# Optimization experiments

Hardware: AMD Instinct MI355X
Metric: run time of the kernel (lower is better)

The kernel has to match this reference:

```python
import jax, jax.numpy as jnp
import numpy as np

D_MODEL, N_LEVELS, N_HEADS, N_POINTS = 256, 4, 8, 4
SHAPES = [(100, 100), (50, 50), (25, 25), (13, 13)]  # (H, W) per level


def setup_inputs() -> dict:
    key = jax.random.key(0)
    ks = jax.random.split(key, 8)
    N = 2
    C = D_MODEL
    Len_in = sum(h * w for h, w in SHAPES)
    Lq = Len_in  # encoder self-attention
    query = jax.random.normal(ks[0], (N, Lq, C), jnp.float32)
    reference_points = jax.random.uniform(ks[1], (N, Lq, N_LEVELS, 2), dtype=jnp.float32)
    input_flatten = jax.random.normal(ks[2], (N, Len_in, C), jnp.float32)
    input_spatial_shapes = np.array(SHAPES, dtype=np.int64)
    areas = input_spatial_shapes[:, 0] * input_spatial_shapes[:, 1]
    input_level_start_index = np.concatenate([[0], np.cumsum(areas)[:-1]]).astype(np.int64)
    s = 1.0 / np.sqrt(C)
    Wv = jax.random.uniform(ks[3], (C, C), jnp.float32, -s, s)
    bv = jnp.zeros((C,), jnp.float32)
    # sampling_offsets: small random weight + the module's grid bias init
    Woff = jax.random.normal(ks[4], (N_HEADS * N_LEVELS * N_POINTS * 2, C), jnp.float32) * 0.01
    thetas = jnp.arange(N_HEADS, dtype=jnp.float32) * (2.0 * np.pi / N_HEADS)
    grid = jnp.stack([jnp.cos(thetas), jnp.sin(thetas)], -1)  # (M,2)
    grid = grid / jnp.max(jnp.abs(grid), axis=-1, keepdims=True)
    grid = jnp.tile(grid[:, None, None, :], (1, N_LEVELS, N_POINTS, 1))
    grid = grid * (jnp.arange(N_POINTS, dtype=jnp.float32) + 1.0)[None, None, :, None]
    boff = grid.reshape(-1)
    Wa = jax.random.normal(ks[5], (N_HEADS * N_LEVELS * N_POINTS, C), jnp.float32) * 0.02
    ba = jnp.zeros((N_HEADS * N_LEVELS * N_POINTS,), jnp.float32)
    Wo = jax.random.uniform(ks[6], (C, C), jnp.float32, -s, s)
    bo = jnp.zeros((C,), jnp.float32)
    return {
        'query': query, 'reference_points': reference_points, 'input_flatten': input_flatten,
        'input_spatial_shapes': input_spatial_shapes, 'input_level_start_index': input_level_start_index,
        'Wv': Wv, 'bv': bv, 'Woff': Woff, 'boff': boff, 'Wa': Wa, 'ba': ba, 'Wo': Wo, 'bo': bo,
    }


def _msda_forward(query, reference_points, input_flatten, shapes, starts,
                  Wv, bv, Woff, boff, Wa, ba, Wo, bo):
    N, Lq, C = query.shape
    M, L, P = N_HEADS, N_LEVELS, N_POINTS
    D = C // M
    value = (input_flatten @ Wv.T + bv).reshape(N, -1, M, D)  # (N, Len_in, M, D)
    off = (query @ Woff.T + boff).reshape(N, Lq, M, L, P, 2)
    attn = jax.nn.softmax((query @ Wa.T + ba).reshape(N, Lq, M, L * P), axis=-1)
    attn = attn.reshape(N, Lq, M, L, P)
    # offset_normalizer = (W_l, H_l)
    norm = jnp.asarray(shapes[:, ::-1].copy(), jnp.float32)  # (L, 2)
    loc = reference_points[:, :, None, :, None, :] + off / norm[None, None, None, :, None, :]
    grids = 2.0 * loc - 1.0  # (N, Lq, M, L, P, 2), grid_sample convention
    out = jnp.zeros((N, Lq, M, D), query.dtype)
    for l in range(L):
        H, W = int(shapes[l, 0]), int(shapes[l, 1])
        s0 = int(starts[l])
        v = value[:, s0:s0 + H * W]  # (N, H*W, M, D)
        # align_corners=False unnormalization
        gx = ((grids[:, :, :, l, :, 0] + 1.0) * W - 1.0) / 2.0  # (N, Lq, M, P)
        gy = ((grids[:, :, :, l, :, 1] + 1.0) * H - 1.0) / 2.0
        x0 = jnp.floor(gx); y0 = jnp.floor(gy)
        fx = gx - x0;       fy = gy - y0
        x0i = x0.astype(jnp.int32); y0i = y0.astype(jnp.int32)

        def gather(iy, ix):
            valid = (iy >= 0) & (iy < H) & (ix >= 0) & (ix < W)
            lin = jnp.clip(iy, 0, H - 1) * W + jnp.clip(ix, 0, W - 1)  # (N, Lq, M, P)
            lin2 = lin.transpose(0, 1, 3, 2).reshape(N, Lq * P, M)
            g = jnp.take_along_axis(v, lin2[..., None], axis=1)  # (N, Lq*P, M, D)
            g = g.reshape(N, Lq, P, M, D).transpose(0, 1, 3, 2, 4)  # (N, Lq, M, P, D)
            return g * valid[..., None]  # zero padding outside

        s00 = gather(y0i, x0i)
        s01 = gather(y0i, x0i + 1)
        s10 = gather(y0i + 1, x0i)
        s11 = gather(y0i + 1, x0i + 1)
        sampled = (s00 * ((1 - fy) * (1 - fx))[..., None] + s01 * ((1 - fy) * fx)[..., None]
                   + s10 * (fy * (1 - fx))[..., None] + s11 * (fy * fx)[..., None])
        out = out + jnp.einsum('nqmp,nqmpd->nqmd', attn[:, :, :, l], sampled)
    out = out.reshape(N, Lq, C)
    return out @ Wo.T + bo


def reference(query, reference_points, input_flatten, input_spatial_shapes, input_level_start_index,
              Wv, bv, Woff, boff, Wa, ba, Wo, bo):
    shapes = np.asarray(input_spatial_shapes)
    starts = np.asarray(input_level_start_index)
    return _msda_forward(query, reference_points, input_flatten, shapes, starts,
                         Wv, bv, Woff, boff, Wa, ba, Wo, bo)
```

## Files before the change

### kernel.cpp

```cpp
#include <hip/hip_runtime.h>
#include <math.h>

#define NB   2
#define LQ   13294
#define NROWS (NB*LQ)
#define CDIM 256
#define HSLICES (NROWS + 1)
#define HS32 ((size_t)HSLICES * 32)

typedef unsigned short u16;
typedef unsigned int   u32;
typedef short bf16x8 __attribute__((ext_vector_type(8)));
typedef float f32x4  __attribute__((ext_vector_type(4)));
typedef float f32x2  __attribute__((ext_vector_type(2)));

struct alignas(8) U16x4 { u16 x, y, z, w; };

__device__ __forceinline__ u16 f2bf(float f) {
    u32 u = __builtin_bit_cast(u32, f);
    u += 0x7FFFu + ((u >> 16) & 1u);
    return (u16)(u >> 16);
}

__device__ __forceinline__ void gload_lds16(const void* g, void* l) {
    __builtin_amdgcn_global_load_lds(
        (__attribute__((address_space(1))) void*)g,
        (__attribute__((address_space(3))) void*)l, 16, 0, 0);
}

__device__ __forceinline__ f32x2 bfpair(u32 u) {
    union { u32 w[2]; f32x2 v; } x;
    x.w[0] = u << 16;
    x.w[1] = u & 0xFFFF0000u;
    return x.v;
}

__global__ __launch_bounds__(256)
void prep_all(const float4* __restrict__ query, const float4* __restrict__ inflat,
              const float* __restrict__ Wv, const float* __restrict__ Woff,
              const float* __restrict__ Wa, const float* __restrict__ Wo,
              u16* __restrict__ qb, u16* __restrict__ ib,
              u16* __restrict__ wb) {
    const int b = blockIdx.x;
    const int t = threadIdx.x;
    if (b < 6647) {
        int i = b * 256 + t;
        float4 v = query[i];
        U16x4 o{f2bf(v.x), f2bf(v.y), f2bf(v.z), f2bf(v.w)};
        *(U16x4*)&qb[(size_t)i * 4] = o;
    } else if (b < 13294) {
        int i = (b - 6647) * 256 + t;
        float4 v = inflat[i];
        U16x4 o{f2bf(v.x), f2bf(v.y), f2bf(v.z), f2bf(v.w)};
        *(U16x4*)&ib[(size_t)i * 4] = o;
    } else {
        int i = (b - 13294) * 256 + t;
        float v;
        if      (i <  65536) v = Wv[i];
        else if (i < 131072) v = Woff[i - 65536];
        else if (i < 163840) v = Wa[i - 131072];
        else                 v = Wo[i - 163840];
        wb[i] = f2bf(v);
    }
}

__device__ __forceinline__ void gemm_core128(
    const u16* __restrict__ A, const u16* __restrict__ Bw, int M, int row0,
    u16* As, u16* Bs, f32x4 (&acc)[4][4]) {
    const int tid  = threadIdx.x;
    const int lane = tid & 63;
    const int wave = tid >> 6;
    const int ln16 = lane & 15;
    const int kq   = lane >> 4;
    const int wr   = (wave >> 1) * 64;
    const int wc   = (wave & 1) * 64;

    #pragma unroll
    for (int kt = 0; kt < 4; ++kt) {
        const int k0 = kt * 64;
        #pragma unroll
        for (int it = 0; it < 4; ++it) {
            int chunk = it * 256 + tid;
            int row = chunk >> 3;
            int ch  = chunk & 7;
            int chs = (ch ^ (row & 7)) * 8;
            int gra = min(row0 + row, M - 1);
            gload_lds16(A  + (size_t)gra * 256 + k0 + chs, As + chunk * 8);
            gload_lds16(Bw + (size_t)row * 256 + k0 + chs, Bs + chunk * 8);
        }
        __syncthreads();
        #pragma unroll
        for (int kf = 0; kf < 2; ++kf) {
            const int ck = kf * 4 + kq;
            bf16x8 a[4], b[4];
            #pragma unroll
            for (int i = 0; i < 4; ++i) {
                int r = wr + i * 16 + ln16;
                a[i] = *(const bf16x8*)&As[r * 64 + ((ck ^ (r & 7)) * 8)];
                int c = wc + i * 16 + ln16;
                b[i] = *(const bf16x8*)&Bs[c * 64 + ((ck ^ (c & 7)) * 8)];
            }
            #pragma unroll
            for (int i = 0; i < 4; ++i)
                #pragma unroll
                for (int j = 0; j < 4; ++j)
                    acc[i][j] = __builtin_amdgcn_mfma_f32_16x16x32_bf16(
                        a[i], b[j], acc[i][j], 0, 0, 0);
        }
        __syncthreads();
    }
}

__global__ __launch_bounds__(256, 4)
void gemm_front(const u16* __restrict__ qb, const u16* __restrict__ ib,
                const u16* __restrict__ wb, const float* __restrict__ bv,
                const float* __restrict__ boff, const float* __restrict__ ba,
                u16* __restrict__ value, float* __restrict__ offb,
                float* __restrict__ logit, int M) {
    __shared__ u16 Sh[128 * 128];
    u16* As = Sh;
    u16* Bs = Sh + 8192;
    const int s    = blockIdx.x;
    const int row0 = blockIdx.y * 128;
    const u16* A  = (s < 2) ? ib : qb;
    const u16* Bw = wb + (size_t)s * 32768;
    const float* bias = (s == 0) ? bv
                      : (s == 1) ? bv + 128
                      : (s == 2) ? boff
                      : (s == 3) ? boff + 128
                      : ba;

    f32x4 acc[4][4] = {};
    gemm_core128(A, Bw, M, row0, As, Bs, acc);

    const int tid  = threadIdx.x;
    const int lane = tid & 63;
    const int wave = tid >> 6;
    const int ln16 = lane & 15, kq = lane >> 4;
    const int wr = (wave >> 1) * 64, wc = (wave & 1) * 64;

    if (s < 2) {
        #pragma unroll
        for (int j = 0; j < 4; ++j) {
            int cl = wc + j * 16 + ln16;
            float bj = bias[cl];
            #pragma unroll
            for (int i = 0; i < 4; ++i)
                #pragma unroll
                for (int r = 0; r < 4; ++r) {
                    int rl = wr + i * 16 + kq * 4 + r;
                    Sh[rl * 128 + cl] = f2bf(acc[i][j][r] + bj);
                }
        }
        __syncthreads();
        #pragma unroll
        for (int it = 0; it < 8; ++it) {
            int ci = it * 256 + tid;
            int tr = ci >> 4;
            int cc = ci & 15;
            int gr = row0 + tr;
            if (gr < M) {
                int cg = s * 128 + cc * 8;
                u16* dst = value + (size_t)(cg >> 5) * HS32
                                 + (size_t)gr * 32 + (cg & 31);
                *(uint4*)dst = *(const uint4*)&Sh[tr * 128 + cc * 8];
            }
        }
        if (s == 0 && blockIdx.y == 0) {
            value[(size_t)(tid >> 5) * HS32 + (size_t)NROWS * 32 + (tid & 31)] = 0;
        }
    } else {
        #pragma unroll
        for (int j = 0; j < 4; ++j) {
            int lc = wc + j * 16 + ln16;
            float bj = bias[lc];
            #pragma unroll
            for (int i = 0; i < 4; ++i) {
                #pragma unroll
                for (int r = 0; r < 4; ++r) {
                    int gr = row0 + wr + i * 16 + kq * 4 + r;
                    if (gr < M) {
                        float o = acc[i][j][r] + bj;
                        if (s < 4)
                            offb[(size_t)gr * 256 + (s - 2) * 128 + lc] = o;
                        else
                            logit[(size_t)gr * 128 + lc] = o;
                    }
                }
            }
        }
    }
}

__global__ __launch_bounds__(256, 4)
void gemm_out(const u16* __restrict__ A, const u16* __restrict__ Bw0,
              const float* __restrict__ bias, float* __restrict__ C, int M) {
    __shared__ u16 Sh[128 * 128];
    u16* As = Sh;
    u16* Bs = Sh + 8192;
    const int s    = blockIdx.x;
    const int row0 = blockIdx.y * 128;
    const u16* Bw = Bw0 + (size_t)s * 32768;

    f32x4 acc[4][4] = {};
    gemm_core128(A, Bw, M, row0, As, Bs, acc);

    const int lane = threadIdx.x & 63;
    const int wave = threadIdx.x >> 6;
    const int ln16 = lane & 15, kq = lane >> 4;
    const int wr = (wave >> 1) * 64, wc = (wave & 1) * 64;
    #pragma unroll
    for (int j = 0; j < 4; ++j) {
        int gc = s * 128 + wc + j * 16 + ln16;
        float bj = bias[gc];
        #pragma unroll
        for (int i = 0; i < 4; ++i) {
            #pragma unroll
            for (int r = 0; r < 4; ++r) {
                int gr = row0 + wr + i * 16 + kq * 4 + r;
                if (gr < M) C[(size_t)gr * 256 + gc] = acc[i][j][r] + bj;
            }
        }
    }
}

__global__ __launch_bounds__(256)
void msda_sample(const u16* __restrict__ value,
                 const float* __restrict__ refpts,
                 const float* __restrict__ off,
                 const float* __restrict__ logits,
                 u16* __restrict__ tmp) {
    __shared__ float sAw[4][8][16];
    __shared__ int   sLin[4][8][16][2];
    __shared__ float sW[4][8][16][4];

    const int t  = threadIdx.x;
    const int qb = blockIdx.x * 4;

    if (t < 32) {
        const int qi = t >> 3, m = t & 7;
        const float* lg = logits + (size_t)(qb + qi) * 128 + m * 16;
        float e[16];
        float mx = -1e30f;
        #pragma unroll
        for (int i = 0; i < 16; ++i) { e[i] = lg[i]; mx = fmaxf(mx, e[i]); }
        float s = 0.f;
        #pragma unroll
        for (int i = 0; i < 16; ++i) { e[i] = __expf(e[i] - mx); s += e[i]; }
        const float inv = 1.f / s;
        #pragma unroll
        for (int i = 0; i < 16; ++i) sAw[qi][m][i] = e[i] * inv;
    }
    __syncthreads();

    #pragma unroll
    for (int j2 = 0; j2 < 2; ++j2) {
        const int job = t + j2 * 256;
        const int qi = job >> 7;
        const int m  = (job >> 4) & 7;
        const int p  = job & 15;
        const int l  = p >> 2, pp = p & 3;
        const int q  = qb + qi;
        const int n  = (q >= LQ) ? 1 : 0;

        const int W = (l == 0) ? 100 : (l == 1) ? 50 : (l == 2) ? 25 : 13;
        const int H = W;
        const int st = (l == 0) ? 0 : (l == 1) ? 10000 : (l == 2) ? 12500 : 13125;
        const float invW = (l == 0) ? 0.01f : (l == 1) ? 0.02f
                         : (l == 2) ? 0.04f : (1.f / 13.f);

        const float rx = refpts[(size_t)q * 8 + l * 2 + 0];
        const float ry = refpts[(size_t)q * 8 + l * 2 + 1];
        const float ox = off[(size_t)q * 256 + m * 32 + (l * 4 + pp) * 2 + 0];
        const float oy = off[(size_t)q * 256 + m * 32 + (l * 4 + pp) * 2 + 1];

        const float locx = rx + ox * invW;
        const float locy = ry + oy * invW;
        const float grx = 2.f * locx - 1.f;
        const float gry = 2.f * locy - 1.f;
        const float gx = ((grx + 1.f) * (float)W - 1.f) * 0.5f;
        const float gy = ((gry + 1.f) * (float)H - 1.f) * 0.5f;
        const float x0f = floorf(gx), y0f = floorf(gy);
        const float fx = gx - x0f, fy = gy - y0f;
        const int x0 = (int)x0f, y0 = (int)y0f;
        const int x1 = x0 + 1, y1 = y0 + 1;

        const int cx0 = min(max(x0, 0), W - 1);
        const int cy0 = min(max(y0, 0), H - 1);
        const int cy1 = min(max(y1, 0), H - 1);
        const bool vx0 = (x0 >= 0) & (x0 < W);
        const bool vx1 = (x1 >= 0) & (x1 < W);
        const bool vy0 = (y0 >= 0) & (y0 < H);
        const bool vy1 = (y1 >= 0) & (y1 < H);

        const float aw = sAw[qi][m][p];
        const int base = n * LQ + st;
        const float w00 = (vy0 & vx0) ? aw * (1.f - fy) * (1.f - fx) : 0.f;
        const float w01 = (vy0 & vx1) ? aw * (1.f - fy) * fx         : 0.f;
        const float w10 = (vy1 & vx0) ? aw * fy * (1.f - fx)         : 0.f;
        const float w11 = (vy1 & vx1) ? aw * fy * fx                 : 0.f;
        const bool fold = (x0 < 0);
        sLin[qi][m][p][0] = base + cy0 * W + cx0;
        sLin[qi][m][p][1] = base + cy1 * W + cx0;
        sW[qi][m][p][0] = fold ? w01 : w00;
        sW[qi][m][p][1] = fold ? 0.f : w01;
        sW[qi][m][p][2] = fold ? w11 : w10;
        sW[qi][m][p][3] = fold ? 0.f : w11;
    }
    __syncthreads();

    const int qi = t >> 6;
    const int m  = (t >> 3) & 7;
    const int e  = t & 7;
    const int xh = e >> 2;
    const int c4 = e & 3;
    const int q  = qb + qi;
    const char* vb = (const char*)value + (size_t)m * (HS32 * 2);
    const u32 eoff = (u32)e * 16u;

    f32x2 a2[4] = {{0.f, 0.f}, {0.f, 0.f}, {0.f, 0.f}, {0.f, 0.f}};
    #pragma unroll
    for (int p = 0; p < 16; ++p) {
        int2   rb = *(const int2*)  &sLin[qi][m][p][0];
        float4 w4 = *(const float4*)&sW  [qi][m][p][0];
        uint4 r0 = *(const uint4*)(vb + ((u32)rb.x * 64u + eoff));
        uint4 r1 = *(const uint4*)(vb + ((u32)rb.y * 64u + eoff));
        const float wa = xh ? w4.y : w4.x;
        const float wb_ = xh ? w4.w : w4.z;
        f32x2 wa2 = {wa, wa};
        f32x2 wb2 = {wb_, wb_};
        a2[0] += wa2 * bfpair(r0.x); a2[1] += wa2 * bfpair(r0.y);
        a2[2] += wa2 * bfpair(r0.z); a2[3] += wa2 * bfpair(r0.w);
        a2[0] += wb2 * bfpair(r1.x); a2[1] += wb2 * bfpair(r1.y);
        a2[2] += wb2 * bfpair(r1.z); a2[3] += wb2 * bfpair(r1.w);
    }
    #pragma unroll
    for (int k = 0; k < 4; ++k) {
        a2[k].x += __shfl_xor(a2[k].x, 4);
        a2[k].y += __shfl_xor(a2[k].y, 4);
    }
    if (xh == 0) {
        uint4 o;
        o.x = (u32)f2bf(a2[0].x) | ((u32)f2bf(a2[0].y) << 16);
        o.y = (u32)f2bf(a2[1].x) | ((u32)f2bf(a2[1].y) << 16);
        o.z = (u32)f2bf(a2[2].x) | ((u32)f2bf(a2[2].y) << 16);
        o.w = (u32)f2bf(a2[3].x) | ((u32)f2bf(a2[3].y) << 16);
        *(uint4*)((char*)tmp + ((u32)q * 512u + (u32)m * 64u + (u32)c4 * 16u)) = o;
    }
}

extern "C" void kernel_launch(void* const* d_in, const int* in_sizes, int n_in,
                              void* d_out, int out_size, void* d_ws, size_t ws_size,
                              hipStream_t stream) {
    const float* query  = (const float*)d_in[0];
    const float* refpts = (const float*)d_in[1];
    const float* inflat = (const float*)d_in[2];
    const float* Wv   = (const float*)d_in[5];
    const float* bv   = (const float*)d_in[6];
    const float* Woff = (const float*)d_in[7];
    const float* boff = (const float*)d_in[8];
    const float* Wa   = (const float*)d_in[9];
    const float* ba   = (const float*)d_in[10];
    const float* Wo   = (const float*)d_in[11];
    const float* bo   = (const float*)d_in[12];
    float* out = (float*)d_out;

    char* ws = (char*)d_ws;
    constexpr size_t SZ16  = (size_t)NROWS * 256 * 2;
    constexpr size_t SZVAL = ((size_t)HSLICES * 512 + 4095) & ~(size_t)4095;
    constexpr size_t SZ32  = (size_t)NROWS * 256 * 4;
    constexpr size_t SZL   = (size_t)NROWS * 128 * 4;
    u16*   qb    = (u16*)(ws);
    u16*   ib    = (u16*)(ws + SZ16);
    u16*   value = (u16*)(ws + 2 * SZ16);
    float* offb  = (float*)(ws + 2 * SZ16 + SZVAL);
    float* logit = (float*)(ws + 2 * SZ16 + SZVAL + SZ32);
    u16*   wb    = (u16*)(ws + 2 * SZ16 + SZVAL + SZ32 + SZL);
    u16*   tmp   = qb;

    const int RG = (NROWS + 127) / 128;

    hipLaunchKernelGGL(prep_all, dim3(14190), dim3(256), 0, stream,
                       (const float4*)query, (const float4*)inflat,
                       Wv, Woff, Wa, Wo, qb, ib, wb);

    gemm_front<<<dim3(5, RG), dim3(256), 0, stream>>>(
        qb, ib, wb, bv, boff, ba, value, offb, logit, NROWS);

    hipLaunchKernelGGL(msda_sample, dim3(NROWS / 4), dim3(256), 0, stream,
                       value, refpts, offb, logit, tmp);

    gemm_out<<<dim3(2, RG), dim3(256), 0, stream>>>(
        tmp, wb + 163840, bo, out, NROWS);
}
```

Before: 208.8 us.

## Remap GEMM blocks per XCD, software-pipeline sampling gathers, pad LDS arrays

Both GEMMs now use a flat 1D grid, with block IDs remapped so that each XCD handles a contiguous range of 26 row groups. This keeps A-tile reuse within one XCD's L2. Launch bounds change: the GEMMs go from 4 to 3 blocks per CU and the sampler gets a bound of 4. The sampling loop double-buffers its gathers, loading point p+1 while accumulating point p, to hide memory latency. The LDS arrays are padded from 16 to 17 entries to change the bank mapping, at the risk of higher register pressure.

Measured after the change: 216.7 us. +3.8%, slower.

```diff
diff --git a/kernel.cpp b/kernel.cpp
--- a/kernel.cpp
+++ b/kernel.cpp
@@ -111,7 +111,7 @@
     }
 }
 
-__global__ __launch_bounds__(256, 4)
+__global__ __launch_bounds__(256, 3)
 void gemm_front(const u16* __restrict__ qb, const u16* __restrict__ ib,
                 const u16* __restrict__ wb, const float* __restrict__ bv,
                 const float* __restrict__ boff, const float* __restrict__ ba,
@@ -120,8 +120,12 @@
     __shared__ u16 Sh[128 * 128];
     u16* As = Sh;
     u16* Bs = Sh + 8192;
-    const int s    = blockIdx.x;
-    const int row0 = blockIdx.y * 128;
+    const int lid  = blockIdx.x;
+    const int xcd  = lid & 7;
+    const int idx  = lid >> 3;
+    const int rg   = xcd * 26 + idx / 5;
+    const int s    = idx % 5;
+    const int row0 = rg * 128;
     const u16* A  = (s < 2) ? ib : qb;
     const u16* Bw = wb + (size_t)s * 32768;
     const float* bias = (s == 0) ? bv
@@ -166,7 +170,7 @@
                 *(uint4*)dst = *(const uint4*)&Sh[tr * 128 + cc * 8];
             }
         }
-        if (s == 0 && blockIdx.y == 0) {
+        if (s == 0 && rg == 0) {
             value[(size_t)(tid >> 5) * HS32 + (size_t)NROWS * 32 + (tid & 31)] = 0;
         }
     } else {
@@ -192,14 +196,18 @@
     }
 }
 
-__global__ __launch_bounds__(256, 4)
+__global__ __launch_bounds__(256, 3)
 void gemm_out(const u16* __restrict__ A, const u16* __restrict__ Bw0,
               const float* __restrict__ bias, float* __restrict__ C, int M) {
     __shared__ u16 Sh[128 * 128];
     u16* As = Sh;
     u16* Bs = Sh + 8192;
-    const int s    = blockIdx.x;
-    const int row0 = blockIdx.y * 128;
+    const int lid  = blockIdx.x;
+    const int xcd  = lid & 7;
+    const int idx  = lid >> 3;
+    const int rg   = xcd * 26 + idx / 2;
+    const int s    = idx % 2;
+    const int row0 = rg * 128;
     const u16* Bw = Bw0 + (size_t)s * 32768;
 
     f32x4 acc[4][4] = {};
@@ -224,15 +232,15 @@
     }
 }
 
-__global__ __launch_bounds__(256)
+__global__ __launch_bounds__(256, 4)
 void msda_sample(const u16* __restrict__ value,
                  const float* __restrict__ refpts,
                  const float* __restrict__ off,
                  const float* __restrict__ logits,
                  u16* __restrict__ tmp) {
     __shared__ float sAw[4][8][16];
-    __shared__ int   sLin[4][8][16][2];
-    __shared__ float sW[4][8][16][4];
+    __shared__ int   sLin[4][8][17][2];
+    __shared__ float sW[4][8][17][4];
 
     const int t  = threadIdx.x;
     const int qb = blockIdx.x * 4;
@@ -319,20 +327,32 @@
     const u32 eoff = (u32)e * 16u;
 
     f32x2 a2[4] = {{0.f, 0.f}, {0.f, 0.f}, {0.f, 0.f}, {0.f, 0.f}};
+
+    int2   rbA = *(const int2*)  &sLin[qi][m][0][0];
+    float4 w4A = *(const float4*)&sW  [qi][m][0][0];
+    uint4  rA0 = *(const uint4*)(vb + ((u32)rbA.x * 64u + eoff));
+    uint4  rA1 = *(const uint4*)(vb + ((u32)rbA.y * 64u + eoff));
+
     #pragma unroll
     for (int p = 0; p < 16; ++p) {
-        int2   rb = *(const int2*)  &sLin[qi][m][p][0];
-        float4 w4 = *(const float4*)&sW  [qi][m][p][0];
-        uint4 r0 = *(const uint4*)(vb + ((u32)rb.x * 64u + eoff));
-        uint4 r1 = *(const uint4*)(vb + ((u32)rb.y * 64u + eoff));
-        const float wa = xh ? w4.y : w4.x;
-        const float wb_ = xh ? w4.w : w4.z;
+        int2   rbB; float4 w4B; uint4 rB0, rB1;
+        if (p < 15) {
+            rbB = *(const int2*)  &sLin[qi][m][p + 1][0];
+            w4B = *(const float4*)&sW  [qi][m][p + 1][0];
+            rB0 = *(const uint4*)(vb + ((u32)rbB.x * 64u + eoff));
+            rB1 = *(const uint4*)(vb + ((u32)rbB.y * 64u + eoff));
+        } else {
+            rbB = rbA; w4B = w4A; rB0 = rA0; rB1 = rA1;
+        }
+        const float wa  = xh ? w4A.y : w4A.x;
+        const float wb_ = xh ? w4A.w : w4A.z;
         f32x2 wa2 = {wa, wa};
         f32x2 wb2 = {wb_, wb_};
-        a2[0] += wa2 * bfpair(r0.x); a2[1] += wa2 * bfpair(r0.y);
-        a2[2] += wa2 * bfpair(r0.z); a2[3] += wa2 * bfpair(r0.w);
-        a2[0] += wb2 * bfpair(r1.x); a2[1] += wb2 * bfpair(r1.y);
-        a2[2] += wb2 * bfpair(r1.z); a2[3] += wb2 * bfpair(r1.w);
+        a2[0] += wa2 * bfpair(rA0.x); a2[1] += wa2 * bfpair(rA0.y);
+        a2[2] += wa2 * bfpair(rA0.z); a2[3] += wa2 * bfpair(rA0.w);
+        a2[0] += wb2 * bfpair(rA1.x); a2[1] += wb2 * bfpair(rA1.y);
+        a2[2] += wb2 * bfpair(rA1.z); a2[3] += wb2 * bfpair(rA1.w);
+        rbA = rbB; w4A = w4B; rA0 = rB0; rA1 = rB1;
     }
     #pragma unroll
     for (int k = 0; k < 4; ++k) {
@@ -378,18 +398,16 @@
     u16*   wb    = (u16*)(ws + 2 * SZ16 + SZVAL + SZ32 + SZL);
     u16*   tmp   = qb;
 
-    const int RG = (NROWS + 127) / 128;
-
     hipLaunchKernelGGL(prep_all, dim3(14190), dim3(256), 0, stream,
                        (const float4*)query, (const float4*)inflat,
                        Wv, Woff, Wa, Wo, qb, ib, wb);
 
-    gemm_front<<<dim3(5, RG), dim3(256), 0, stream>>>(
+    gemm_front<<<dim3(1040), dim3(256), 0, stream>>>(
         qb, ib, wb, bv, boff, ba, value, offb, logit, NROWS);
 
     hipLaunchKernelGGL(msda_sample, dim3(NROWS / 4), dim3(256), 0, stream,
                        value, refpts, offb, logit, tmp);
 
-    gemm_out<<<dim3(2, RG), dim3(256), 0, stream>>>(
+    gemm_out<<<dim3(416), dim3(256), 0, stream>>>(
         tmp, wb + 163840, bo, out, NROWS);
 }
```
